# Kernel optimization log

Hardware: AMD Instinct MI355X
Metric: run time of the kernel (lower is better)

Reference implementation:

```python
import jax, jax.numpy as jnp
import numpy as np

N, E, D, H, C = 100000, 1600000, 128, 256, 40


def setup_inputs() -> dict:
    key = jax.random.key(0)
    ks = jax.random.split(key, 10)
    x = jax.random.normal(ks[0], (N, D), dtype=jnp.float32)
    src = jax.random.randint(ks[1], (E,), 0, N, dtype=jnp.int32)
    dst = jax.random.randint(ks[2], (E,), 0, N, dtype=jnp.int32)
    # GIN layer 1 MLP (bias-free), kaiming-uniform-like scale 1/sqrt(fan_in)
    w1a = jax.random.normal(ks[3], (D, H), dtype=jnp.float32) / np.sqrt(D)
    w1b = jax.random.normal(ks[4], (H, H), dtype=jnp.float32) / np.sqrt(H)
    # GIN layer 2 MLP
    w2a = jax.random.normal(ks[5], (H, H), dtype=jnp.float32) / np.sqrt(H)
    w2b = jax.random.normal(ks[6], (H, H), dtype=jnp.float32) / np.sqrt(H)
    # eps initialized to 0 per reset_parameters
    eps1 = jnp.zeros((), dtype=jnp.float32)
    eps2 = jnp.zeros((), dtype=jnp.float32)
    # final classifier fc (with bias)
    fc_w = jax.random.normal(ks[7], (H, C), dtype=jnp.float32) / np.sqrt(H)
    fc_b = jax.random.normal(ks[8], (C,), dtype=jnp.float32) * 0.01
    return {"x": x, "src": src, "dst": dst,
            "eps1": eps1, "w1a": w1a, "w1b": w1b,
            "eps2": eps2, "w2a": w2a, "w2b": w2b,
            "fc_w": fc_w, "fc_b": fc_b}


def reference(x, src, dst, eps1, w1a, w1b, eps2, w2a, w2b, fc_w, fc_b):
    n = x.shape[0]

    def gin_layer(h, eps, wa, wb):
        # GINConv sum-aggregation: scatter-add neighbor feats over edges
        agg = jax.ops.segment_sum(h[src], dst, num_segments=n)  # [N, d]
        rst = (1.0 + eps) * h + agg
        # 2-layer bias-free MLP with ReLU between
        return jax.nn.relu(rst @ wa) @ wb

    h = jax.nn.relu(gin_layer(x, eps1, w1a, w1b))   # layer + outer activation
    h = jax.nn.relu(gin_layer(h, eps2, w2a, w2b))   # dropout p=0 -> identity
    return h @ fc_w + fc_b                           # [N, C]
```

## Files before the change

kernel.cpp:

```cpp
#include <hip/hip_runtime.h>

#define N_NODES 100000
#define NPAD    100032
#define N_EDGES 1600000
#define DIM_IN  128
#define DIM_H   256
#define DIM_C   40

#define NB   391
#define NBLK 391
#define CHUNK 4096
#define ECAP 6144

#define CVT_BLOCKS 25000
#define WCVT_BLOCKS 1280

typedef unsigned short bf16_t;
typedef __attribute__((ext_vector_type(8))) short short8;
typedef __attribute__((ext_vector_type(4))) float f32x4;

__device__ __forceinline__ bf16_t f2b(float f) {
    unsigned int u = __float_as_uint(f);
    unsigned int r = (u + 0x7fffu + ((u >> 16) & 1u)) >> 16;
    return (bf16_t)r;
}

__device__ __forceinline__ void gl_lds16(const void* gsrc, void* ldst) {
    __builtin_amdgcn_global_load_lds(
        (const __attribute__((address_space(1))) void*)gsrc,
        (__attribute__((address_space(3))) void*)ldst,
        16, 0, 0);
}


__global__ __launch_bounds__(256) void k_prep(
    const int* __restrict__ dst, int* __restrict__ cnt2,
    const float* __restrict__ x, signed char* __restrict__ x8, float* __restrict__ xs,
    const float* __restrict__ w1a, const float* __restrict__ w1b,
    const float* __restrict__ w2a, const float* __restrict__ w2b,
    const float* __restrict__ fcw,
    bf16_t* __restrict__ o1a, bf16_t* __restrict__ o1b,
    bf16_t* __restrict__ o2a, bf16_t* __restrict__ o2b, bf16_t* __restrict__ ofc,
    int* __restrict__ ticket)
{
    __shared__ int h[NB];
    int blk = blockIdx.x, t = threadIdx.x;

    if (blk < NBLK) {
        if (blk == 0 && t == 0) *ticket = 0;
        for (int i = t; i < NB; i += 256) h[i] = 0;
        __syncthreads();
        int base = blk * CHUNK;
        int end = min(base + CHUNK, N_EDGES);
        for (int i = base + t; i < end; i += 256)
            atomicAdd(&h[dst[i] >> 8], 1);
        __syncthreads();
        for (int i = t; i < NB; i += 256) cnt2[blk * NB + i] = h[i];
        return;
    }
    blk -= NBLK;

    if (blk < CVT_BLOCKS) {
        int gid = blk * 256 + t;
        int u = gid >> 6, lane = gid & 63;
        float2 v = *(const float2*)(x + (size_t)u * 128 + lane * 2);
        float m = fmaxf(fabsf(v.x), fabsf(v.y));
        #pragma unroll
        for (int d = 1; d < 64; d <<= 1)
            m = fmaxf(m, __shfl_xor(m, d, 64));
        float inv = (m > 0.f) ? 127.f / m : 0.f;
        int q0 = (int)rintf(v.x * inv);
        int q1 = (int)rintf(v.y * inv);
        unsigned short pk = (unsigned short)((q0 & 0xff) | ((q1 & 0xff) << 8));
        *(unsigned short*)(x8 + ((unsigned)u << 7) + lane * 2) = pk;
        if (lane == 0) xs[u] = (m > 0.f) ? m * (1.f / 127.f) : 0.f;
        return;
    }
    blk -= CVT_BLOCKS;

    int r = blk >> 8;
    int idx = (blk & 255) * 256 + t;
    const float* in; bf16_t* out; int K, N, Npad;
    switch (r) {
        case 0: in = w1a; out = o1a; K = 128; N = 256; Npad = 256; break;
        case 1: in = w1b; out = o1b; K = 256; N = 256; Npad = 256; break;
        case 2: in = w2a; out = o2a; K = 256; N = 256; Npad = 256; break;
        case 3: in = w2b; out = o2b; K = 256; N = 256; Npad = 256; break;
        default: in = fcw; out = ofc; K = 256; N = 40;  Npad = 64;  break;
    }
    if (idx >= Npad * K) return;
    int n = idx / K, k = idx - n * K;
    float v = (n < N) ? in[(size_t)k * N + n] : 0.f;
    int kstep = k >> 5, quad = (k >> 3) & 3, e = k & 7;
    int tt = n >> 4, l15 = n & 15;
    size_t opos = (size_t)kstep * (Npad * 32) + ((size_t)(tt * 64 + quad * 16 + l15)) * 8 + e;
    out[opos] = f2b(v);
}


__global__ void k_bscanA(const int* __restrict__ cnt2, int* __restrict__ basep,
                         int* __restrict__ btot, int* __restrict__ ticket,
                         int* __restrict__ boff) {
    __shared__ int s[512];
    __shared__ int isLast;
    int t = threadIdx.x, b = blockIdx.x;
    int v = (t < NBLK) ? cnt2[t * NB + b] : 0;
    s[t] = v;
    __syncthreads();
    #pragma unroll
    for (int d = 1; d < 512; d <<= 1) {
        int tv = (t >= d) ? s[t - d] : 0;
        __syncthreads();
        s[t] += tv;
        __syncthreads();
    }
    if (t < NBLK) basep[t * NB + b] = s[t] - v;
    if (t == 511) atomicExch(&btot[b], s[511]);
    __syncthreads();
    if (t == 0) {
        __threadfence();
        int old = atomicAdd(ticket, 1);
        isLast = (old == NB - 1);
    }
    __syncthreads();
    if (!isLast) return;

    __threadfence();
    int v2 = (t < NB) ? atomicAdd(&btot[t], 0) : 0;
    s[t] = v2;
    __syncthreads();
    #pragma unroll
    for (int d = 1; d < 512; d <<= 1) {
        int tv = (t >= d) ? s[t - d] : 0;
        __syncthreads();
        s[t] += tv;
        __syncthreads();
    }
    if (t < NB) boff[t] = s[t] - v2;
    if (t == NB - 1) boff[NB] = s[t];
}

__global__ void k_bscatter(const int* __restrict__ src, const int* __restrict__ dst,
                           const int* __restrict__ basep, const int* __restrict__ boff,
                           int* __restrict__ ebuf, int e) {
    __shared__ int cur[NB];
    int t = threadIdx.x, blk = blockIdx.x;
    for (int i = t; i < NB; i += 256) cur[i] = basep[blk * NB + i] + boff[i];
    __syncthreads();
    int base = blk * CHUNK;
    int end = min(base + CHUNK, e);
    for (int i = base + t; i < end; i += 256) {
        int sv = src[i], dv = dst[i];
        int pos = atomicAdd(&cur[dv >> 8], 1);
        ebuf[pos] = sv | ((dv & 255) << 24);
    }
}

__global__ __launch_bounds__(256) void k_build(const int* __restrict__ ebuf,
                                               const int* __restrict__ boff,
                                               int* __restrict__ off,
                                               int* __restrict__ csr) {
    __shared__ int ec[ECAP];
    __shared__ int h[256];
    __shared__ int cur[256];
    int t = threadIdx.x, b = blockIdx.x;
    int node0 = b << 8;
    int e0 = boff[b], e1 = boff[b + 1];
    int ne = e1 - e0;
    bool fits = (ne <= ECAP);
    h[t] = 0;
    __syncthreads();
    if (fits) {
        for (int i = t; i < ne; i += 256) {
            int p = ebuf[e0 + i];
            ec[i] = p;
            atomicAdd(&h[(unsigned)p >> 24], 1);
        }
    } else {
        for (int i = t; i < ne; i += 256)
            atomicAdd(&h[(unsigned)ebuf[e0 + i] >> 24], 1);
    }
    __syncthreads();
    int mydeg = h[t];
    #pragma unroll
    for (int d = 1; d < 256; d <<= 1) {
        int tv = (t >= d) ? h[t - d] : 0;
        __syncthreads();
        h[t] += tv;
        __syncthreads();
    }
    int node = node0 + t;
    if (node < N_NODES) off[node + 1] = e0 + h[t];
    if (b == 0 && t == 0) off[0] = 0;
    cur[t] = e0 + h[t] - mydeg;
    __syncthreads();
    if (fits) {
        for (int i = t; i < ne; i += 256) {
            int p = ec[i];
            int pos = atomicAdd(&cur[(unsigned)p >> 24], 1);
            csr[pos] = p & 0xFFFFFF;
        }
    } else {
        for (int i = t; i < ne; i += 256) {
            int p = ebuf[e0 + i];
            int pos = atomicAdd(&cur[(unsigned)p >> 24], 1);
            csr[pos] = p & 0xFFFFFF;
        }
    }
}


__global__ void k_agg_i8(const signed char* __restrict__ h8, const float* __restrict__ hs,
                         const int* __restrict__ off, const int* __restrict__ csr,
                         const float* __restrict__ eps_p,
                         bf16_t* __restrict__ rst, int n) {
    int gid = blockIdx.x * blockDim.x + threadIdx.x;
    int u = __builtin_amdgcn_readfirstlane(gid >> 6);
    int lane = threadIdx.x & 63;
    if (u >= n) return;

    float acc0 = 0.f, acc1 = 0.f;
    int r0 = off[u], r1 = off[u + 1];
    unsigned loff = lane * 2u;

    for (int base = r0; base < r1; base += 64) {
        int m = r1 - base; if (m > 64) m = 64;
        int li = (lane < m) ? lane : (m - 1);
        int iv = csr[base + li];
        for (int c = 0; c < m; c += 16) {
            int s[16]; float sc[16]; unsigned v[16];
            #pragma unroll
            for (int t = 0; t < 16; t++)
                s[t] = __builtin_amdgcn_readlane(iv, c + t);
            #pragma unroll
            for (int t = 0; t < 16; t++)
                sc[t] = (c + t < m) ? hs[s[t]] : 0.f;
            #pragma unroll
            for (int t = 0; t < 16; t++)
                v[t] = *(const unsigned short*)(h8 + (((unsigned)s[t] << 7) + loff));
            #pragma unroll
            for (int t = 0; t < 16; t++) {
                acc0 += (float)(int)(signed char)(v[t] & 0xffu) * sc[t];
                acc1 += (float)(int)(signed char)(v[t] >> 8) * sc[t];
            }
        }
    }

    float scu = hs[u] * (1.0f + eps_p[0]);
    unsigned vu = *(const unsigned short*)(h8 + (((unsigned)u << 7) + loff));
    float o0 = (float)(int)(signed char)(vu & 0xffu) * scu + acc0;
    float o1 = (float)(int)(signed char)(vu >> 8) * scu + acc1;

    int R = u >> 6, rr = u & 63;
    int i4 = rr >> 4, l15v = rr & 15;
    int ks = lane >> 4, quad = (lane >> 2) & 3, e2 = (lane & 3) * 2;
    size_t pos = (((size_t)R * 4 + ks) * 256 + (size_t)(i4 * 64 + quad * 16 + l15v)) * 8 + e2;
    *(unsigned int*)(rst + pos) =
        (unsigned int)f2b(o0) | ((unsigned int)f2b(o1) << 16);
}


__global__ void k_agg_u8(const unsigned char* __restrict__ h8,
                         const float* __restrict__ hs,
                         const int* __restrict__ off, const int* __restrict__ csr,
                         const float* __restrict__ eps_p,
                         bf16_t* __restrict__ rst, int n) {
    int gid = blockIdx.x * blockDim.x + threadIdx.x;
    int u = __builtin_amdgcn_readfirstlane(gid >> 6);
    int lane = threadIdx.x & 63;
    if (u >= n) return;

    float acc[4] = {0.f, 0.f, 0.f, 0.f};
    int r0 = off[u], r1 = off[u + 1];
    unsigned loff = lane * 4u;

    for (int base = r0; base < r1; base += 64) {
        int m = r1 - base; if (m > 64) m = 64;
        int li = (lane < m) ? lane : (m - 1);
        int iv = csr[base + li];
        for (int c = 0; c < m; c += 16) {
            int s[16]; float sc[16]; unsigned int v[16];
            #pragma unroll
            for (int t = 0; t < 16; t++)
                s[t] = __builtin_amdgcn_readlane(iv, c + t);
            #pragma unroll
            for (int t = 0; t < 16; t++)
                sc[t] = (c + t < m) ? hs[s[t]] : 0.f;
            #pragma unroll
            for (int t = 0; t < 16; t++)
                v[t] = *(const unsigned int*)(h8 + (((unsigned)s[t] << 8) + loff));
            #pragma unroll
            for (int t = 0; t < 16; t++) {
                acc[0] += (float)(v[t] & 0xffu) * sc[t];
                acc[1] += (float)((v[t] >> 8) & 0xffu) * sc[t];
                acc[2] += (float)((v[t] >> 16) & 0xffu) * sc[t];
                acc[3] += (float)(v[t] >> 24) * sc[t];
            }
        }
    }

    float ep = 1.0f + eps_p[0];
    unsigned int vu = *(const unsigned int*)(h8 + (((unsigned)u << 8) + loff));
    float scu = hs[u] * ep;
    float o0 = (float)(vu & 0xffu) * scu + acc[0];
    float o1 = (float)((vu >> 8) & 0xffu) * scu + acc[1];
    float o2 = (float)((vu >> 16) & 0xffu) * scu + acc[2];
    float o3 = (float)(vu >> 24) * scu + acc[3];
    uint2 ov;
    ov.x = (unsigned int)f2b(o0) | ((unsigned int)f2b(o1) << 16);
    ov.y = (unsigned int)f2b(o2) | ((unsigned int)f2b(o3) << 16);

    int R = u >> 6, rr = u & 63;
    int i4 = rr >> 4, l15v = rr & 15;
    int ks = lane >> 3, quad = (lane >> 1) & 3, e4 = (lane & 1) * 4;
    size_t pos = (((size_t)R * 8 + ks) * 256 + (size_t)(i4 * 64 + quad * 16 + l15v)) * 8 + e4;
    *(uint2*)(rst + pos) = ov;
}


#define TS_STRIDE 264

template <int K1, bool OUT8, bool FUSE_FC>
__global__ __launch_bounds__(256, 2) void k_mlp(
    const bf16_t* __restrict__ A, const bf16_t* __restrict__ W1t,
    const bf16_t* __restrict__ W2t, bf16_t* __restrict__ H,
    unsigned char* __restrict__ H8, float* __restrict__ Hs,
    const bf16_t* __restrict__ FCt, const float* __restrict__ fc_b,
    float* __restrict__ Cout, int M)
{
    constexpr int NS1 = K1 / 32;
    __shared__ __align__(16) bf16_t As[2][64 * 32];
    __shared__ __align__(16) bf16_t Bs[2][256 * 32];
    __shared__ __align__(16) bf16_t Ts[64 * TS_STRIDE];
    __shared__ int rmax[64];

    int tid = threadIdx.x;
    int wave = tid >> 6, lane = tid & 63;
    int l15 = lane & 15, quad = lane >> 4;
    int bm = blockIdx.x * 64;

    auto stageA = [&](int kstep, int b) {
        gl_lds16(A + ((size_t)blockIdx.x * NS1 + kstep) * 2048 + tid * 8, &As[b][tid * 8]);
    };
    auto stageB = [&](const bf16_t* W, int kstep, int b) {
        #pragma unroll
        for (int l = 0; l < 4; l++) {
            int c = l * 256 + tid;
            gl_lds16(W + ((size_t)kstep * 1024 + c) * 8, &Bs[b][c * 8]);
        }
    };

    f32x4 acc[4][4];
    #pragma unroll
    for (int i = 0; i < 4; i++)
        #pragma unroll
        for (int j = 0; j < 4; j++) acc[i][j] = 0.f;

    stageA(0, 0); stageB(W1t, 0, 0);
    #pragma unroll
    for (int k = 0; k < NS1; k++) {
        int cur = k & 1;
        if (k + 1 < NS1) {
            stageA(k + 1, cur ^ 1); stageB(W1t, k + 1, cur ^ 1);
            asm volatile("s_waitcnt vmcnt(5)" ::: "memory");
        } else {
            asm volatile("s_waitcnt vmcnt(0)" ::: "memory");
        }
        __builtin_amdgcn_sched_barrier(0);
        __builtin_amdgcn_s_barrier();

        short8 af[4], bfv[4];
        #pragma unroll
        for (int i = 0; i < 4; i++)
            af[i] = *(const short8*)&As[cur][(i * 64 + lane) * 8];
        #pragma unroll
        for (int j = 0; j < 4; j++)
            bfv[j] = *(const short8*)&Bs[cur][((wave * 4 + j) * 64 + lane) * 8];

        #pragma unroll
        for (int i = 0; i < 4; i++)
            #pragma unroll
            for (int j = 0; j < 4; j++)
                acc[i][j] = __builtin_amdgcn_mfma_f32_16x16x32_bf16(af[i], bfv[j], acc[i][j], 0, 0, 0);

        asm volatile("s_waitcnt lgkmcnt(0)" ::: "memory");
        __builtin_amdgcn_sched_barrier(0);
        __builtin_amdgcn_s_barrier();
    }

    int wn = wave * 64;
    #pragma unroll
    for (int i = 0; i < 4; i++)
        #pragma unroll
        for (int j = 0; j < 4; j++) {
            int row = i * 16 + quad * 4;
            int col = wn + j * 16 + l15;
            #pragma unroll
            for (int r = 0; r < 4; r++)
                Ts[(row + r) * TS_STRIDE + col] = f2b(fmaxf(acc[i][j][r], 0.f));
        }

    #pragma unroll
    for (int i = 0; i < 4; i++)
        #pragma unroll
        for (int j = 0; j < 4; j++) acc[i][j] = 0.f;
    __syncthreads();

    stageB(W2t, 0, 0);
    #pragma unroll
    for (int k = 0; k < 8; k++) {
        int cur = k & 1;
        if (k + 1 < 8) {
            stageB(W2t, k + 1, cur ^ 1);
            asm volatile("s_waitcnt vmcnt(4)" ::: "memory");
        } else {
            asm volatile("s_waitcnt vmcnt(0)" ::: "memory");
        }
        __builtin_amdgcn_sched_barrier(0);
        __builtin_amdgcn_s_barrier();

        short8 af[4], bfv[4];
        #pragma unroll
        for (int i = 0; i < 4; i++)
            af[i] = *(const short8*)&Ts[(i * 16 + l15) * TS_STRIDE + k * 32 + quad * 8];
        #pragma unroll
        for (int j = 0; j < 4; j++)
            bfv[j] = *(const short8*)&Bs[cur][((wave * 4 + j) * 64 + lane) * 8];

        #pragma unroll
        for (int i = 0; i < 4; i++)
            #pragma unroll
            for (int j = 0; j < 4; j++)
                acc[i][j] = __builtin_amdgcn_mfma_f32_16x16x32_bf16(af[i], bfv[j], acc[i][j], 0, 0, 0);

        asm volatile("s_waitcnt lgkmcnt(0)" ::: "memory");
        __builtin_amdgcn_sched_barrier(0);
        __builtin_amdgcn_s_barrier();
    }

    if constexpr (OUT8) {
        if (tid < 64) rmax[tid] = 0;
        __syncthreads();
        #pragma unroll
        for (int i = 0; i < 4; i++)
            #pragma unroll
            for (int r = 0; r < 4; r++) {
                float m = 0.f;
                #pragma unroll
                for (int j = 0; j < 4; j++) m = fmaxf(m, acc[i][j][r]);
                atomicMax(&rmax[i * 16 + quad * 4 + r], __float_as_int(m));
            }
        __syncthreads();
        #pragma unroll
        for (int i = 0; i < 4; i++) {
            #pragma unroll
            for (int r = 0; r < 4; r++) {
                int row = i * 16 + quad * 4 + r;
                int rowg = bm + row;
                if (rowg >= M) continue;
                float rm = __int_as_float(rmax[row]);
                float inv = (rm > 0.f) ? 255.f / rm : 0.f;
                #pragma unroll
                for (int j = 0; j < 4; j++) {
                    int col = wn + j * 16 + l15;
                    float v = fmaxf(acc[i][j][r], 0.f);
                    unsigned q = (unsigned)(v * inv + 0.5f);
                    if (q > 255u) q = 255u;
                    H8[(size_t)rowg * 256 + col] = (unsigned char)q;
                }
                if (wave == 0 && l15 == 0)
                    Hs[rowg] = rm * (1.f / 255.f);
            }
        }
    } else if constexpr (FUSE_FC) {
        #pragma unroll
        for (int i = 0; i < 4; i++)
            #pragma unroll
            for (int j = 0; j < 4; j++) {
                int row = i * 16 + quad * 4;
                int col = wn + j * 16 + l15;
                #pragma unroll
                for (int r = 0; r < 4; r++)
                    Ts[(row + r) * TS_STRIDE + col] = f2b(fmaxf(acc[i][j][r], 0.f));
            }
        __syncthreads();

        f32x4 acc3[3];
        #pragma unroll
        for (int j = 0; j < 3; j++) acc3[j] = 0.f;

        auto stage3 = [&](int kstep, int b) {
            gl_lds16(FCt + ((size_t)kstep * 256 + tid) * 8, &Bs[b][tid * 8]);
        };

        stage3(0, 0);
        #pragma unroll
        for (int k = 0; k < 8; k++) {
            int cur = k & 1;
            if (k + 1 < 8) {
                stage3(k + 1, cur ^ 1);
                asm volatile("s_waitcnt vmcnt(1)" ::: "memory");
            } else {
                asm volatile("s_waitcnt vmcnt(0)" ::: "memory");
            }
            __builtin_amdgcn_sched_barrier(0);
            __builtin_amdgcn_s_barrier();

            short8 af = *(const short8*)&Ts[(wave * 16 + l15) * TS_STRIDE + k * 32 + quad * 8];
            #pragma unroll
            for (int j = 0; j < 3; j++) {
                short8 bfv = *(const short8*)&Bs[cur][((j * 64) + lane) * 8];
                acc3[j] = __builtin_amdgcn_mfma_f32_16x16x32_bf16(af, bfv, acc3[j], 0, 0, 0);
            }

            asm volatile("s_waitcnt lgkmcnt(0)" ::: "memory");
            __builtin_amdgcn_sched_barrier(0);
            __builtin_amdgcn_s_barrier();
        }

        #pragma unroll
        for (int j = 0; j < 3; j++) {
            int col = j * 16 + l15;
            if (col >= DIM_C) continue;
            float bv = fc_b[col];
            #pragma unroll
            for (int r = 0; r < 4; r++) {
                int rowg = bm + wave * 16 + quad * 4 + r;
                if (rowg < M)
                    Cout[(size_t)rowg * DIM_C + col] = acc3[j][r] + bv;
            }
        }
    } else {
        #pragma unroll
        for (int j = 0; j < 4; j++) {
            int col = wn + j * 16 + l15;
            #pragma unroll
            for (int i = 0; i < 4; i++) {
                #pragma unroll
                for (int r = 0; r < 4; r++) {
                    int rowg = bm + i * 16 + quad * 4 + r;
                    if (rowg < M)
                        H[(size_t)rowg * 256 + col] = f2b(fmaxf(acc[i][j][r], 0.f));
                }
            }
        }
    }
}


static inline size_t rnd256(size_t x) { return (x + 255) & ~(size_t)255; }

extern "C" void kernel_launch(void* const* d_in, const int* in_sizes, int n_in,
                              void* d_out, int out_size, void* d_ws, size_t ws_size,
                              hipStream_t stream) {
    const float* x    = (const float*)d_in[0];
    const int*   src  = (const int*)d_in[1];
    const int*   dst  = (const int*)d_in[2];
    const float* eps1 = (const float*)d_in[3];
    const float* w1a  = (const float*)d_in[4];
    const float* w1b  = (const float*)d_in[5];
    const float* eps2 = (const float*)d_in[6];
    const float* w2a  = (const float*)d_in[7];
    const float* w2b  = (const float*)d_in[8];
    const float* fc_w = (const float*)d_in[9];
    const float* fc_b = (const float*)d_in[10];
    float* out = (float*)d_out;

    char* w = (char*)d_ws;
    int* off  = (int*)w; w += rnd256(sizeof(int) * (size_t)(N_NODES + 1));
    int* csr  = (int*)w; w += rnd256(sizeof(int) * (size_t)N_EDGES);
    int* cnt2  = (int*)w; w += rnd256(sizeof(int) * (size_t)NBLK * NB);
    int* basep = (int*)w; w += rnd256(sizeof(int) * (size_t)NBLK * NB);
    int* btot  = (int*)w; w += rnd256(sizeof(int) * 512);
    int* boff  = (int*)w; w += rnd256(sizeof(int) * (NB + 1));
    bf16_t* w1a_t = (bf16_t*)w; w += rnd256(2 * (size_t)DIM_H * DIM_IN);
    bf16_t* w1b_t = (bf16_t*)w; w += rnd256(2 * (size_t)DIM_H * DIM_H);
    bf16_t* w2a_t = (bf16_t*)w; w += rnd256(2 * (size_t)DIM_H * DIM_H);
    bf16_t* w2b_t = (bf16_t*)w; w += rnd256(2 * (size_t)DIM_H * DIM_H);
    bf16_t* fc_t  = (bf16_t*)w; w += rnd256(2 * (size_t)128 * DIM_H);
    signed char* x8 = (signed char*)w; w += rnd256((size_t)N_NODES * DIM_IN);
    float* xs = (float*)w; w += rnd256(sizeof(float) * (size_t)N_NODES);
    unsigned char* h8 = (unsigned char*)w; w += rnd256((size_t)N_NODES * DIM_H);
    float* hs = (float*)w; w += rnd256(sizeof(float) * (size_t)N_NODES);
    bf16_t* R12 = (bf16_t*)w; w += rnd256(2 * (size_t)NPAD * DIM_H);
    bf16_t* R3  = (bf16_t*)w; w += rnd256(2 * (size_t)NPAD * DIM_H);

    bf16_t* rst1 = R12;
    int* ebuf = (int*)R3;
    int* ticket = btot + 500;

    k_prep<<<NBLK + CVT_BLOCKS + WCVT_BLOCKS, 256, 0, stream>>>(
        dst, cnt2, x, x8, xs, w1a, w1b, w2a, w2b, fc_w,
        w1a_t, w1b_t, w2a_t, w2b_t, fc_t, ticket);

    k_bscanA<<<NB, 512, 0, stream>>>(cnt2, basep, btot, ticket, boff);
    k_bscatter<<<NBLK, 256, 0, stream>>>(src, dst, basep, boff, ebuf, N_EDGES);
    k_build<<<NB, 256, 0, stream>>>(ebuf, boff, off, csr);

    const int agg_blocks = (N_NODES * 64 + 255) / 256;
    const int mlp_blocks = NPAD / 64;

    k_agg_i8<<<agg_blocks, 256, 0, stream>>>(x8, xs, off, csr, eps1, rst1, N_NODES);
    k_mlp<DIM_IN, true, false><<<mlp_blocks, 256, 0, stream>>>(
        rst1, w1a_t, w1b_t, nullptr, h8, hs, nullptr, nullptr, nullptr, N_NODES);

    k_agg_u8<<<agg_blocks, 256, 0, stream>>>(h8, hs, off, csr, eps2, (bf16_t*)R3, N_NODES);
    k_mlp<DIM_H, false, true><<<mlp_blocks, 256, 0, stream>>>(
        (bf16_t*)R3, w2a_t, w2b_t, nullptr, nullptr, nullptr, fc_t, fc_b, out, N_NODES);
}
```

Baseline: 410.8 us.

## Split MLP tile across 8 waves and store hidden tile in MFMA fragment layout

The fused MLP kernel moves from 256 to 512 threads per block. Each wave now owns 32 output columns instead of 64, which halves the per-wave accumulator registers and targets higher occupancy (launch bounds 512,4). The intermediate hidden tile in LDS is relaid out into MFMA A-fragment order, so the second GEMM reads it with contiguous 16-byte loads instead of padded-stride row reads. Wait counts for A/B staging are adjusted per thread group, and the FC stage now runs on only half the waves, leaving the others idle at barriers.

```diff
diff --git a/kernel.cpp b/kernel.cpp
--- a/kernel.cpp
+++ b/kernel.cpp
@@ -318,10 +318,8 @@
 }
 
 
-#define TS_STRIDE 264
-
 template <int K1, bool OUT8, bool FUSE_FC>
-__global__ __launch_bounds__(256, 2) void k_mlp(
+__global__ __launch_bounds__(512, 4) void k_mlp(
     const bf16_t* __restrict__ A, const bf16_t* __restrict__ W1t,
     const bf16_t* __restrict__ W2t, bf16_t* __restrict__ H,
     unsigned char* __restrict__ H8, float* __restrict__ Hs,
@@ -331,30 +329,37 @@
     constexpr int NS1 = K1 / 32;
     __shared__ __align__(16) bf16_t As[2][64 * 32];
     __shared__ __align__(16) bf16_t Bs[2][256 * 32];
-    __shared__ __align__(16) bf16_t Ts[64 * TS_STRIDE];
+    __shared__ __align__(16) bf16_t Ts[64 * 256];
     __shared__ int rmax[64];
 
     int tid = threadIdx.x;
     int wave = tid >> 6, lane = tid & 63;
     int l15 = lane & 15, quad = lane >> 4;
     int bm = blockIdx.x * 64;
+    int wn = wave * 32;
 
     auto stageA = [&](int kstep, int b) {
-        gl_lds16(A + ((size_t)blockIdx.x * NS1 + kstep) * 2048 + tid * 8, &As[b][tid * 8]);
+        if (tid < 256)
+            gl_lds16(A + ((size_t)blockIdx.x * NS1 + kstep) * 2048 + tid * 8, &As[b][tid * 8]);
     };
     auto stageB = [&](const bf16_t* W, int kstep, int b) {
         #pragma unroll
-        for (int l = 0; l < 4; l++) {
-            int c = l * 256 + tid;
+        for (int l = 0; l < 2; l++) {
+            int c = l * 512 + tid;
             gl_lds16(W + ((size_t)kstep * 1024 + c) * 8, &Bs[b][c * 8]);
         }
     };
 
-    f32x4 acc[4][4];
+    auto ts_el = [&](int row, int col) {
+        return ((col >> 5) * 4 + (row >> 4)) * 512 +
+               ((((col >> 3) & 3) * 16) + (row & 15)) * 8 + (col & 7);
+    };
+
+    f32x4 acc[4][2];
     #pragma unroll
     for (int i = 0; i < 4; i++)
         #pragma unroll
-        for (int j = 0; j < 4; j++) acc[i][j] = 0.f;
+        for (int j = 0; j < 2; j++) acc[i][j] = 0.f;
 
     stageA(0, 0); stageB(W1t, 0, 0);
     #pragma unroll
@@ -362,25 +367,26 @@
         int cur = k & 1;
         if (k + 1 < NS1) {
             stageA(k + 1, cur ^ 1); stageB(W1t, k + 1, cur ^ 1);
-            asm volatile("s_waitcnt vmcnt(5)" ::: "memory");
+            if (tid < 256) { asm volatile("s_waitcnt vmcnt(3)" ::: "memory"); }
+            else           { asm volatile("s_waitcnt vmcnt(2)" ::: "memory"); }
         } else {
             asm volatile("s_waitcnt vmcnt(0)" ::: "memory");
         }
         __builtin_amdgcn_sched_barrier(0);
         __builtin_amdgcn_s_barrier();
 
-        short8 af[4], bfv[4];
+        short8 af[4], bfv[2];
         #pragma unroll
         for (int i = 0; i < 4; i++)
             af[i] = *(const short8*)&As[cur][(i * 64 + lane) * 8];
         #pragma unroll
-        for (int j = 0; j < 4; j++)
-            bfv[j] = *(const short8*)&Bs[cur][((wave * 4 + j) * 64 + lane) * 8];
+        for (int j = 0; j < 2; j++)
+            bfv[j] = *(const short8*)&Bs[cur][((wave * 2 + j) * 64 + lane) * 8];
 
         #pragma unroll
         for (int i = 0; i < 4; i++)
             #pragma unroll
-            for (int j = 0; j < 4; j++)
+            for (int j = 0; j < 2; j++)
                 acc[i][j] = __builtin_amdgcn_mfma_f32_16x16x32_bf16(af[i], bfv[j], acc[i][j], 0, 0, 0);
 
         asm volatile("s_waitcnt lgkmcnt(0)" ::: "memory");
@@ -388,22 +394,22 @@
         __builtin_amdgcn_s_barrier();
     }
 
-    int wn = wave * 64;
     #pragma unroll
     for (int i = 0; i < 4; i++)
         #pragma unroll
-        for (int j = 0; j < 4; j++) {
-            int row = i * 16 + quad * 4;
+        for (int j = 0; j < 2; j++) {
             int col = wn + j * 16 + l15;
             #pragma unroll
-            for (int r = 0; r < 4; r++)
-                Ts[(row + r) * TS_STRIDE + col] = f2b(fmaxf(acc[i][j][r], 0.f));
+            for (int r = 0; r < 4; r++) {
+                int row = i * 16 + quad * 4 + r;
+                Ts[ts_el(row, col)] = f2b(fmaxf(acc[i][j][r], 0.f));
+            }
         }
 
     #pragma unroll
     for (int i = 0; i < 4; i++)
         #pragma unroll
-        for (int j = 0; j < 4; j++) acc[i][j] = 0.f;
+        for (int j = 0; j < 2; j++) acc[i][j] = 0.f;
     __syncthreads();
 
     stageB(W2t, 0, 0);
@@ -412,25 +418,25 @@
         int cur = k & 1;
         if (k + 1 < 8) {
             stageB(W2t, k + 1, cur ^ 1);
-            asm volatile("s_waitcnt vmcnt(4)" ::: "memory");
+            asm volatile("s_waitcnt vmcnt(2)" ::: "memory");
         } else {
             asm volatile("s_waitcnt vmcnt(0)" ::: "memory");
         }
         __builtin_amdgcn_sched_barrier(0);
         __builtin_amdgcn_s_barrier();
 
-        short8 af[4], bfv[4];
+        short8 af[4], bfv[2];
         #pragma unroll
         for (int i = 0; i < 4; i++)
-            af[i] = *(const short8*)&Ts[(i * 16 + l15) * TS_STRIDE + k * 32 + quad * 8];
-        #pragma unroll
-        for (int j = 0; j < 4; j++)
-            bfv[j] = *(const short8*)&Bs[cur][((wave * 4 + j) * 64 + lane) * 8];
+            af[i] = *(const short8*)&Ts[((k * 4 + i) * 64 + lane) * 8];
+        #pragma unroll
+        for (int j = 0; j < 2; j++)
+            bfv[j] = *(const short8*)&Bs[cur][((wave * 2 + j) * 64 + lane) * 8];
 
         #pragma unroll
         for (int i = 0; i < 4; i++)
             #pragma unroll
-            for (int j = 0; j < 4; j++)
+            for (int j = 0; j < 2; j++)
                 acc[i][j] = __builtin_amdgcn_mfma_f32_16x16x32_bf16(af[i], bfv[j], acc[i][j], 0, 0, 0);
 
         asm volatile("s_waitcnt lgkmcnt(0)" ::: "memory");
@@ -447,7 +453,7 @@
             for (int r = 0; r < 4; r++) {
                 float m = 0.f;
                 #pragma unroll
-                for (int j = 0; j < 4; j++) m = fmaxf(m, acc[i][j][r]);
+                for (int j = 0; j < 2; j++) m = fmaxf(m, acc[i][j][r]);
                 atomicMax(&rmax[i * 16 + quad * 4 + r], __float_as_int(m));
             }
         __syncthreads();
@@ -461,7 +467,7 @@
                 float rm = __int_as_float(rmax[row]);
                 float inv = (rm > 0.f) ? 255.f / rm : 0.f;
                 #pragma unroll
-                for (int j = 0; j < 4; j++) {
+                for (int j = 0; j < 2; j++) {
                     int col = wn + j * 16 + l15;
                     float v = fmaxf(acc[i][j][r], 0.f);
                     unsigned q = (unsigned)(v * inv + 0.5f);
@@ -476,12 +482,13 @@
         #pragma unroll
         for (int i = 0; i < 4; i++)
             #pragma unroll
-            for (int j = 0; j < 4; j++) {
-                int row = i * 16 + quad * 4;
+            for (int j = 0; j < 2; j++) {
                 int col = wn + j * 16 + l15;
                 #pragma unroll
-                for (int r = 0; r < 4; r++)
-                    Ts[(row + r) * TS_STRIDE + col] = f2b(fmaxf(acc[i][j][r], 0.f));
+                for (int r = 0; r < 4; r++) {
+                    int row = i * 16 + quad * 4 + r;
+                    Ts[ts_el(row, col)] = f2b(fmaxf(acc[i][j][r], 0.f));
+                }
             }
         __syncthreads();
 
@@ -490,7 +497,8 @@
         for (int j = 0; j < 3; j++) acc3[j] = 0.f;
 
         auto stage3 = [&](int kstep, int b) {
-            gl_lds16(FCt + ((size_t)kstep * 256 + tid) * 8, &Bs[b][tid * 8]);
+            if (tid < 256)
+                gl_lds16(FCt + ((size_t)kstep * 256 + tid) * 8, &Bs[b][tid * 8]);
         };
 
         stage3(0, 0);
@@ -499,40 +507,43 @@
             int cur = k & 1;
             if (k + 1 < 8) {
                 stage3(k + 1, cur ^ 1);
-                asm volatile("s_waitcnt vmcnt(1)" ::: "memory");
+                if (tid < 256) { asm volatile("s_waitcnt vmcnt(1)" ::: "memory"); }
             } else {
-                asm volatile("s_waitcnt vmcnt(0)" ::: "memory");
+                if (tid < 256) { asm volatile("s_waitcnt vmcnt(0)" ::: "memory"); }
             }
             __builtin_amdgcn_sched_barrier(0);
             __builtin_amdgcn_s_barrier();
 
-            short8 af = *(const short8*)&Ts[(wave * 16 + l15) * TS_STRIDE + k * 32 + quad * 8];
-            #pragma unroll
-            for (int j = 0; j < 3; j++) {
-                short8 bfv = *(const short8*)&Bs[cur][((j * 64) + lane) * 8];
-                acc3[j] = __builtin_amdgcn_mfma_f32_16x16x32_bf16(af, bfv, acc3[j], 0, 0, 0);
-            }
-
-            asm volatile("s_waitcnt lgkmcnt(0)" ::: "memory");
+            if (tid < 256) {
+                short8 af = *(const short8*)&Ts[((k * 4 + wave) * 64 + lane) * 8];
+                #pragma unroll
+                for (int j = 0; j < 3; j++) {
+                    short8 bfv = *(const short8*)&Bs[cur][((j * 64) + lane) * 8];
+                    acc3[j] = __builtin_amdgcn_mfma_f32_16x16x32_bf16(af, bfv, acc3[j], 0, 0, 0);
+                }
+                asm volatile("s_waitcnt lgkmcnt(0)" ::: "memory");
+            }
             __builtin_amdgcn_sched_barrier(0);
             __builtin_amdgcn_s_barrier();
         }
 
-        #pragma unroll
-        for (int j = 0; j < 3; j++) {
-            int col = j * 16 + l15;
-            if (col >= DIM_C) continue;
-            float bv = fc_b[col];
-            #pragma unroll
-            for (int r = 0; r < 4; r++) {
-                int rowg = bm + wave * 16 + quad * 4 + r;
-                if (rowg < M)
-                    Cout[(size_t)rowg * DIM_C + col] = acc3[j][r] + bv;
+        if (tid < 256) {
+            #pragma unroll
+            for (int j = 0; j < 3; j++) {
+                int col = j * 16 + l15;
+                if (col >= DIM_C) continue;
+                float bv = fc_b[col];
+                #pragma unroll
+                for (int r = 0; r < 4; r++) {
+                    int rowg = bm + wave * 16 + quad * 4 + r;
+                    if (rowg < M)
+                        Cout[(size_t)rowg * DIM_C + col] = acc3[j][r] + bv;
+                }
             }
         }
     } else {
         #pragma unroll
-        for (int j = 0; j < 4; j++) {
+        for (int j = 0; j < 2; j++) {
             int col = wn + j * 16 + l15;
             #pragma unroll
             for (int i = 0; i < 4; i++) {
@@ -601,10 +612,10 @@
     const int mlp_blocks = NPAD / 64;
 
     k_agg_i8<<<agg_blocks, 256, 0, stream>>>(x8, xs, off, csr, eps1, rst1, N_NODES);
-    k_mlp<DIM_IN, true, false><<<mlp_blocks, 256, 0, stream>>>(
+    k_mlp<DIM_IN, true, false><<<mlp_blocks, 512, 0, stream>>>(
         rst1, w1a_t, w1b_t, nullptr, h8, hs, nullptr, nullptr, nullptr, N_NODES);
 
     k_agg_u8<<<agg_blocks, 256, 0, stream>>>(h8, hs, off, csr, eps2, (bf16_t*)R3, N_NODES);
-    k_mlp<DIM_H, false, true><<<mlp_blocks, 256, 0, stream>>>(
+    k_mlp<DIM_H, false, true><<<mlp_blocks, 512, 0, stream>>>(
         (bf16_t*)R3, w2a_t, w2b_t, nullptr, nullptr, nullptr, fc_t, fc_b, out, N_NODES);
 }
```

Result: no change. 413.3 us (+0.6%).

## Load MLP GEMM operands directly from global memory and pack hidden tile in fragment order

Applied to the files above, without the earlier changes.

Removes the double-buffered LDS staging of A and weight tiles (and their per-step barriers) so each wave reads MFMA fragments straight from global memory. The intermediate hidden tile is stored in LDS in a fragment-packed layout, so it is read with contiguous 16-byte loads. Launch bounds rise to 4 blocks per CU because LDS use drops. The cost is more global/L2 traffic, since weights are reloaded per wave and not shared through LDS, and there is no explicit prefetch overlap.

```diff
diff --git a/kernel.cpp b/kernel.cpp
--- a/kernel.cpp
+++ b/kernel.cpp
@@ -318,10 +318,8 @@
 }
 
 
-#define TS_STRIDE 264
-
 template <int K1, bool OUT8, bool FUSE_FC>
-__global__ __launch_bounds__(256, 2) void k_mlp(
+__global__ __launch_bounds__(256, 4) void k_mlp(
     const bf16_t* __restrict__ A, const bf16_t* __restrict__ W1t,
     const bf16_t* __restrict__ W2t, bf16_t* __restrict__ H,
     unsigned char* __restrict__ H8, float* __restrict__ Hs,
@@ -329,26 +327,19 @@
     float* __restrict__ Cout, int M)
 {
     constexpr int NS1 = K1 / 32;
-    __shared__ __align__(16) bf16_t As[2][64 * 32];
-    __shared__ __align__(16) bf16_t Bs[2][256 * 32];
-    __shared__ __align__(16) bf16_t Ts[64 * TS_STRIDE];
+    __shared__ __align__(16) bf16_t Ts[64 * 256];
     __shared__ int rmax[64];
 
     int tid = threadIdx.x;
     int wave = tid >> 6, lane = tid & 63;
     int l15 = lane & 15, quad = lane >> 4;
     int bm = blockIdx.x * 64;
-
-    auto stageA = [&](int kstep, int b) {
-        gl_lds16(A + ((size_t)blockIdx.x * NS1 + kstep) * 2048 + tid * 8, &As[b][tid * 8]);
+    int wn = wave * 64;
+
+    auto ts_el = [&](int row, int col) {
+        return ((col >> 5) * 4 + (row >> 4)) * 512 +
+               ((((col >> 3) & 3) * 16) + (row & 15)) * 8 + (col & 7);
     };
-    auto stageB = [&](const bf16_t* W, int kstep, int b) {
-        #pragma unroll
-        for (int l = 0; l < 4; l++) {
-            int c = l * 256 + tid;
-            gl_lds16(W + ((size_t)kstep * 1024 + c) * 8, &Bs[b][c * 8]);
-        }
-    };
 
     f32x4 acc[4][4];
     #pragma unroll
@@ -356,48 +347,33 @@
         #pragma unroll
         for (int j = 0; j < 4; j++) acc[i][j] = 0.f;
 
-    stageA(0, 0); stageB(W1t, 0, 0);
+    const bf16_t* Ab = A + (size_t)blockIdx.x * NS1 * 2048;
     #pragma unroll
     for (int k = 0; k < NS1; k++) {
-        int cur = k & 1;
-        if (k + 1 < NS1) {
-            stageA(k + 1, cur ^ 1); stageB(W1t, k + 1, cur ^ 1);
-            asm volatile("s_waitcnt vmcnt(5)" ::: "memory");
-        } else {
-            asm volatile("s_waitcnt vmcnt(0)" ::: "memory");
-        }
-        __builtin_amdgcn_sched_barrier(0);
-        __builtin_amdgcn_s_barrier();
-
         short8 af[4], bfv[4];
         #pragma unroll
         for (int i = 0; i < 4; i++)
-            af[i] = *(const short8*)&As[cur][(i * 64 + lane) * 8];
+            af[i] = *(const short8*)(Ab + ((size_t)k * 2048 + (i * 64 + lane) * 8));
         #pragma unroll
         for (int j = 0; j < 4; j++)
-            bfv[j] = *(const short8*)&Bs[cur][((wave * 4 + j) * 64 + lane) * 8];
-
+            bfv[j] = *(const short8*)(W1t + ((size_t)k * 1024 + (wave * 4 + j) * 64 + lane) * 8);
         #pragma unroll
         for (int i = 0; i < 4; i++)
             #pragma unroll
             for (int j = 0; j < 4; j++)
                 acc[i][j] = __builtin_amdgcn_mfma_f32_16x16x32_bf16(af[i], bfv[j], acc[i][j], 0, 0, 0);
-
-        asm volatile("s_waitcnt lgkmcnt(0)" ::: "memory");
-        __builtin_amdgcn_sched_barrier(0);
-        __builtin_amdgcn_s_barrier();
-    }
-
-    int wn = wave * 64;
+    }
+
     #pragma unroll
     for (int i = 0; i < 4; i++)
         #pragma unroll
         for (int j = 0; j < 4; j++) {
-            int row = i * 16 + quad * 4;
             int col = wn + j * 16 + l15;
             #pragma unroll
-            for (int r = 0; r < 4; r++)
-                Ts[(row + r) * TS_STRIDE + col] = f2b(fmaxf(acc[i][j][r], 0.f));
+            for (int r = 0; r < 4; r++) {
+                int row = i * 16 + quad * 4 + r;
+                Ts[ts_el(row, col)] = f2b(fmaxf(acc[i][j][r], 0.f));
+            }
         }
 
     #pragma unroll
@@ -406,36 +382,20 @@
         for (int j = 0; j < 4; j++) acc[i][j] = 0.f;
     __syncthreads();
 
-    stageB(W2t, 0, 0);
     #pragma unroll
     for (int k = 0; k < 8; k++) {
-        int cur = k & 1;
-        if (k + 1 < 8) {
-            stageB(W2t, k + 1, cur ^ 1);
-            asm volatile("s_waitcnt vmcnt(4)" ::: "memory");
-        } else {
-            asm volatile("s_waitcnt vmcnt(0)" ::: "memory");
-        }
-        __builtin_amdgcn_sched_barrier(0);
-        __builtin_amdgcn_s_barrier();
-
         short8 af[4], bfv[4];
         #pragma unroll
         for (int i = 0; i < 4; i++)
-            af[i] = *(const short8*)&Ts[(i * 16 + l15) * TS_STRIDE + k * 32 + quad * 8];
+            af[i] = *(const short8*)&Ts[((k * 4 + i) * 64 + lane) * 8];
         #pragma unroll
         for (int j = 0; j < 4; j++)
-            bfv[j] = *(const short8*)&Bs[cur][((wave * 4 + j) * 64 + lane) * 8];
-
+            bfv[j] = *(const short8*)(W2t + ((size_t)k * 1024 + (wave * 4 + j) * 64 + lane) * 8);
         #pragma unroll
         for (int i = 0; i < 4; i++)
             #pragma unroll
             for (int j = 0; j < 4; j++)
                 acc[i][j] = __builtin_amdgcn_mfma_f32_16x16x32_bf16(af[i], bfv[j], acc[i][j], 0, 0, 0);
-
-        asm volatile("s_waitcnt lgkmcnt(0)" ::: "memory");
-        __builtin_amdgcn_sched_barrier(0);
-        __builtin_amdgcn_s_barrier();
     }
 
     if constexpr (OUT8) {
@@ -473,15 +433,17 @@
             }
         }
     } else if constexpr (FUSE_FC) {
+        __syncthreads();
         #pragma unroll
         for (int i = 0; i < 4; i++)
             #pragma unroll
             for (int j = 0; j < 4; j++) {
-                int row = i * 16 + quad * 4;
                 int col = wn + j * 16 + l15;
                 #pragma unroll
-                for (int r = 0; r < 4; r++)
-                    Ts[(row + r) * TS_STRIDE + col] = f2b(fmaxf(acc[i][j][r], 0.f));
+                for (int r = 0; r < 4; r++) {
+                    int row = i * 16 + quad * 4 + r;
+                    Ts[ts_el(row, col)] = f2b(fmaxf(acc[i][j][r], 0.f));
+                }
             }
         __syncthreads();
 
@@ -489,33 +451,14 @@
         #pragma unroll
         for (int j = 0; j < 3; j++) acc3[j] = 0.f;
 
-        auto stage3 = [&](int kstep, int b) {
-            gl_lds16(FCt + ((size_t)kstep * 256 + tid) * 8, &Bs[b][tid * 8]);
-        };
-
-        stage3(0, 0);
         #pragma unroll
         for (int k = 0; k < 8; k++) {
-            int cur = k & 1;
-            if (k + 1 < 8) {
-                stage3(k + 1, cur ^ 1);
-                asm volatile("s_waitcnt vmcnt(1)" ::: "memory");
-            } else {
-                asm volatile("s_waitcnt vmcnt(0)" ::: "memory");
-            }
-            __builtin_amdgcn_sched_barrier(0);
-            __builtin_amdgcn_s_barrier();
-
-            short8 af = *(const short8*)&Ts[(wave * 16 + l15) * TS_STRIDE + k * 32 + quad * 8];
+            short8 af = *(const short8*)&Ts[((k * 4 + wave) * 64 + lane) * 8];
             #pragma unroll
             for (int j = 0; j < 3; j++) {
-                short8 bfv = *(const short8*)&Bs[cur][((j * 64) + lane) * 8];
+                short8 bfv = *(const short8*)(FCt + ((size_t)k * 256 + j * 64 + lane) * 8);
                 acc3[j] = __builtin_amdgcn_mfma_f32_16x16x32_bf16(af, bfv, acc3[j], 0, 0, 0);
             }
-
-            asm volatile("s_waitcnt lgkmcnt(0)" ::: "memory");
-            __builtin_amdgcn_sched_barrier(0);
-            __builtin_amdgcn_s_barrier();
         }
 
         #pragma unroll
```

Result: faster. 390.2 us (-5.0%).
